# Performance work log

Measured on AMD Instinct MI355X. Metric: run time of the kernel, lower is better.

The kernel has to match this reference:

```python
import jax, jax.numpy as jnp
import numpy as np

B, S, D, H, F, E, K = 2, 2048, 1024, 16, 4096, 8, 2


def setup_inputs() -> dict:
    key = jax.random.key(0)
    ks = jax.random.split(key, 10)
    s = 0.02
    return {
        "x": jax.random.normal(ks[0], (B, S, D), jnp.float32),
        "ln_g": jnp.ones((D,), jnp.float32),
        "ln_b": jnp.zeros((D,), jnp.float32),
        "Wq": s * jax.random.normal(ks[1], (D, D), jnp.float32),
        "Wk": s * jax.random.normal(ks[2], (D, D), jnp.float32),
        "Wv": s * jax.random.normal(ks[3], (D, D), jnp.float32),
        "Wo": s * jax.random.normal(ks[4], (D, D), jnp.float32),
        "Wg": s * jax.random.normal(ks[5], (D, E), jnp.float32),
        "W1": s * jax.random.normal(ks[6], (E, D, F), jnp.float32),
        "b1": jnp.zeros((E, F), jnp.float32),
        "W2": s * jax.random.normal(ks[7], (E, F, D), jnp.float32),
        "b2": jnp.zeros((E, D), jnp.float32),
    }


def _layernorm(x, g, b, eps=1e-5):
    m = x.mean(-1, keepdims=True)
    v = x.var(-1, keepdims=True)
    return (x - m) * jax.lax.rsqrt(v + eps) * g + b


def reference(x, ln_g, ln_b, Wq, Wk, Wv, Wo, Wg, W1, b1, W2, b2):
    Bb, Ss, Dd = x.shape
    dh = Dd // H
    # --- pre-norm multi-head self-attention with residual ---
    h = _layernorm(x, ln_g, ln_b)
    q = (h @ Wq).reshape(Bb, Ss, H, dh)
    k = (h @ Wk).reshape(Bb, Ss, H, dh)
    v = (h @ Wv).reshape(Bb, Ss, H, dh)
    scores = jnp.einsum("bqhd,bkhd->bhqk", q, k) / np.sqrt(dh).astype(np.float32)
    attn = jax.nn.softmax(scores, axis=-1)
    o = jnp.einsum("bhqk,bkhd->bqhd", attn, v).reshape(Bb, Ss, Dd) @ Wo
    x = x + o
    # --- top-2 MoE with residual ---
    nE = Wg.shape[-1]
    probs = jax.nn.softmax(x @ Wg, axis=-1)  # [B,S,E]
    topv, topi = jax.lax.top_k(probs, K)
    topv = topv / topv.sum(-1, keepdims=True)
    w = (jax.nn.one_hot(topi, nE, dtype=x.dtype) * topv[..., None]).sum(-2)  # [B,S,E]
    h1 = jax.nn.gelu(jnp.einsum("bsd,edf->besf", x, W1) + b1[None, :, None, :])
    h2 = jnp.einsum("besf,efd->besd", h1, W2) + b2[None, :, None, :]
    out = x + jnp.einsum("bse,besd->bsd", w, h2)
    return out
```

## Files before the change

kernel.cpp:

```cpp
#include <hip/hip_runtime.h>
#include <hip/hip_bf16.h>

constexpr int Sc = 2048;
constexpr int Dc = 1024;
constexpr int Fc = 4096;
constexpr int Ec = 8;
constexpr int NTOK = 4096;

typedef __attribute__((ext_vector_type(8))) short short8;
typedef __attribute__((ext_vector_type(4))) float floatx4;
typedef unsigned short u16;

__device__ __forceinline__ u16 f2bf(float f) {
    __hip_bfloat16 h = __float2bfloat16(f);
    return *reinterpret_cast<u16*>(&h);
}

__device__ __forceinline__ float gelu_fast(float x) {
    float x2 = x * x;
    float z = x * fmaf(-0.07135481282f, x2, -1.5957691216057308f);
    float e = __expf(z);
    return x * __builtin_amdgcn_rcpf(1.0f + e);
}

__device__ __forceinline__ void async16(const u16* g, u16* l) {
    __builtin_amdgcn_global_load_lds(
        (const __attribute__((address_space(1))) unsigned int*)g,
        (__attribute__((address_space(3))) unsigned int*)l, 16, 0, 0);
}

#define BAR() asm volatile("s_barrier" ::: "memory")

__global__ __launch_bounds__(256) void tcast_kernel(const float* __restrict__ src,
                                                    u16* __restrict__ dst,
                                                    int R, int C,
                                                    size_t sstride, size_t dstride) {
    __shared__ float t[64][65];
    const float* s = src + (size_t)blockIdx.z * sstride;
    u16* d = dst + (size_t)blockIdx.z * dstride;
    int r0 = blockIdx.y * 64, c0 = blockIdx.x * 64;
    int tid = threadIdx.x;
#pragma unroll
    for (int i = 0; i < 4; i++) {
        int c = tid + i * 256;
        int row = c >> 4, col4 = (c & 15) * 4;
        float4 v = *(const float4*)(s + (size_t)(r0 + row) * C + c0 + col4);
        t[row][col4 + 0] = v.x;
        t[row][col4 + 1] = v.y;
        t[row][col4 + 2] = v.z;
        t[row][col4 + 3] = v.w;
    }
    __syncthreads();
#pragma unroll
    for (int i = 0; i < 2; i++) {
        int c = tid + i * 256;
        int dr = c >> 3, m8 = (c & 7) * 8;
        union { u16 us[8]; uint4 v; } pk;
#pragma unroll
        for (int j = 0; j < 8; j++) pk.us[j] = f2bf(t[m8 + j][dr]);
        *(uint4*)(d + (size_t)(c0 + dr) * R + r0 + m8) = pk.v;
    }
}

__global__ __launch_bounds__(256) void btrans_kernel(const u16* __restrict__ src,
                                                     u16* __restrict__ dst,
                                                     int R, int C) {
    __shared__ u16 t[64][72];
    int r0 = blockIdx.y * 64, c0 = blockIdx.x * 64;
    int tid = threadIdx.x;
#pragma unroll
    for (int i = 0; i < 2; i++) {
        int c = tid + i * 256;
        int row = c >> 3, s8 = (c & 7) * 8;
        *(uint4*)&t[row][s8] = *(const uint4*)(src + (size_t)(r0 + row) * C + c0 + s8);
    }
    __syncthreads();
#pragma unroll
    for (int i = 0; i < 2; i++) {
        int c = tid + i * 256;
        int row = c >> 3, s8 = (c & 7) * 8;
        union { u16 us[8]; uint4 v; } pk;
#pragma unroll
        for (int j = 0; j < 8; j++) pk.us[j] = t[s8 + j][row];
        *(uint4*)(dst + (size_t)(c0 + row) * R + r0 + s8) = pk.v;
    }
}

__global__ __launch_bounds__(256) void ln_kernel(const float* __restrict__ x,
                                                 const float* __restrict__ g,
                                                 const float* __restrict__ b,
                                                 u16* __restrict__ hb) {
    int row = blockIdx.x, tid = threadIdx.x;
    const float* xr = x + (size_t)row * Dc;
    float4 xv = ((const float4*)xr)[tid];
    float s = xv.x + xv.y + xv.z + xv.w;
    float ss = xv.x * xv.x + xv.y * xv.y + xv.z * xv.z + xv.w * xv.w;
    __shared__ float r1[256], r2[256];
    r1[tid] = s; r2[tid] = ss;
    __syncthreads();
    for (int off = 128; off > 0; off >>= 1) {
        if (tid < off) { r1[tid] += r1[tid + off]; r2[tid] += r2[tid + off]; }
        __syncthreads();
    }
    float mean = r1[0] * (1.0f / Dc);
    float var = r2[0] * (1.0f / Dc) - mean * mean;
    float rs = rsqrtf(var + 1e-5f);
    float4 gv = ((const float4*)g)[tid];
    float4 bv = ((const float4*)b)[tid];
    ushort4 o;
    o.x = f2bf((xv.x - mean) * rs * gv.x + bv.x);
    o.y = f2bf((xv.y - mean) * rs * gv.y + bv.y);
    o.z = f2bf((xv.z - mean) * rs * gv.z + bv.z);
    o.w = f2bf((xv.w - mean) * rs * gv.w + bv.w);
    *(ushort4*)(hb + (size_t)row * Dc + tid * 4) = o;
}

template <int MODE>
__global__ __launch_bounds__(256) void gemm_mfma(
    const u16* __restrict__ A, const u16* __restrict__ BT,
    int N, int K,
    u16* __restrict__ out_q, u16* __restrict__ out_k, u16* __restrict__ out_v,
    const float* __restrict__ resid, float* __restrict__ out_f32,
    u16* __restrict__ out_bf, const float* __restrict__ bias,
    const int* __restrict__ counts, const int* __restrict__ offsets,
    const int* __restrict__ list_tok) {
    const int tid = threadIdx.x;
    const int m0 = blockIdx.y * 128, n0 = blockIdx.x * 128;
    __shared__ u16 As[128][32];
    __shared__ u16 Bs[128][32];
    const u16* Bbase = BT;
    const int w = tid >> 6, lane = tid & 63;
    const int wm = (w >> 1) * 64, wn = (w & 1) * 64;
    const int lr = lane & 15, lq = lane >> 4;

    const int rA0 = w * 32 + (lane >> 2), rA1 = rA0 + 16;
    const int gsegu = (((lane & 3) ^ ((lane >> 3) & 3))) * 8;
    size_t ra0 = (size_t)(m0 + rA0) * K;
    size_t ra1 = (size_t)(m0 + rA1) * K;
    const u16* gA0 = A + ra0 + gsegu;
    const u16* gA1 = A + ra1 + gsegu;
    const u16* gB0 = Bbase + (size_t)(n0 + rA0) * K + gsegu;
    const u16* gB1 = Bbase + (size_t)(n0 + rA1) * K + gsegu;
    u16* ldsA0 = &As[w * 32][0];
    u16* ldsA1 = &As[w * 32 + 16][0];
    u16* ldsB0 = &Bs[w * 32][0];
    u16* ldsB1 = &Bs[w * 32 + 16][0];

    const int fs = (lq ^ ((lr >> 1) & 3)) * 8;
    const u16* apt[4];
    const u16* bpt[4];
#pragma unroll
    for (int i = 0; i < 4; i++) {
        apt[i] = &As[wm + i * 16 + lr][fs];
        bpt[i] = &Bs[wn + i * 16 + lr][fs];
    }

    floatx4 acc[4][4];
#pragma unroll
    for (int i = 0; i < 4; i++)
#pragma unroll
        for (int j = 0; j < 4; j++) acc[i][j] = (floatx4){0.f, 0.f, 0.f, 0.f};

    for (int k0 = 0; k0 < K; k0 += 32) {
        async16(gA0 + k0, ldsA0);
        async16(gA1 + k0, ldsA1);
        async16(gB0 + k0, ldsB0);
        async16(gB1 + k0, ldsB1);
        __syncthreads();
        short8 af[4], bfr[4];
#pragma unroll
        for (int i = 0; i < 4; i++) af[i] = *(const short8*)apt[i];
#pragma unroll
        for (int j = 0; j < 4; j++) bfr[j] = *(const short8*)bpt[j];
#pragma unroll
        for (int i = 0; i < 4; i++)
#pragma unroll
            for (int j = 0; j < 4; j++)
                acc[i][j] = __builtin_amdgcn_mfma_f32_16x16x32_bf16(af[i], bfr[j], acc[i][j], 0, 0, 0);
        __syncthreads();
    }

#pragma unroll
    for (int i = 0; i < 4; i++)
#pragma unroll
        for (int j = 0; j < 4; j++) {
            int col = n0 + wn + j * 16 + lr;
            int row0 = m0 + wm + i * 16 + lq * 4;
#pragma unroll
            for (int r = 0; r < 4; r++) {
                size_t idx = (size_t)(row0 + r) * 1024 + col;
                float v = acc[i][j][r] + resid[idx];
                out_f32[idx] = v;
                out_bf[idx] = f2bf(v);
            }
        }
}

template <int MODE>
__global__ __launch_bounds__(512, 2) void gemm256(
    const u16* __restrict__ A, const u16* __restrict__ BT, int Nn, int Kfull,
    u16* __restrict__ out_q, u16* __restrict__ out_k, u16* __restrict__ out_v,
    u16* __restrict__ out_bf, float* __restrict__ o32a, float* __restrict__ o32b,
    const float* __restrict__ bias,
    const int* __restrict__ counts, const int* __restrict__ offsets,
    const int* __restrict__ list_tok) {
    __shared__ __attribute__((aligned(16))) u16 smem[66048];
    int e = 0, cnt = 0, off = 0, ks = 0;
    const int bm = (int)blockIdx.y;
    const int bn = (int)blockIdx.x;
    if (MODE >= 2) {
        e = (MODE == 3) ? ((int)blockIdx.z >> 1) : (int)blockIdx.z;
        if (MODE == 3) ks = (int)blockIdx.z & 1;
        cnt = counts[e];
        if (bm * 256 >= cnt) return;
        off = offsets[e];
    }
    const int tid = threadIdx.x;
    const int m0 = bm * 256, n0 = bn * 256;
    const int w = tid >> 6, lane = tid & 63;
    const int wm = w >> 2, wn = w & 3;
    const int lr = lane & 15, lq = lane >> 4;
    const int sz8 = (lr & 7) << 3;

    int* toksL = (int*)(smem + 65536);
    if (MODE == 2) {
        if (tid < 256) toksL[tid] = list_tok[off + min(m0 + tid, cnt - 1)];
        __syncthreads();
    }
    const int K = Kfull;
    const int NT = (MODE == 3 ? 2048 : K) / 64;
    const size_t kb = (MODE == 3) ? (size_t)ks * 2048 : 0;
    const u16* Bb = BT + (MODE >= 2 ? (size_t)e * (size_t)Nn * K : (size_t)0);

    const u16* srcA[4];
    const u16* srcB[4];
    {
        const int rl8 = w * 8 + (lane >> 3);
        const int sg = ((lane & 7) ^ (lane >> 3)) * 8;
#pragma unroll
        for (int i = 0; i < 4; i++) {
            int rA = i * 64 + rl8;
            size_t gr;
            if (MODE == 2) gr = (size_t)toksL[rA];
            else if (MODE == 3) gr = (size_t)(off + min(m0 + rA, cnt - 1));
            else gr = (size_t)(m0 + rA);
            srcA[i] = A + gr * K + kb + sg;
            srcB[i] = Bb + (size_t)(n0 + rA) * K + kb + sg;
        }
    }

    short8 areg[4][2], breg[4][2];
    floatx4 acc[8][4];
#pragma unroll
    for (int i = 0; i < 8; i++)
#pragma unroll
        for (int j = 0; j < 4; j++) acc[i][j] = (floatx4){0.f, 0.f, 0.f, 0.f};

#define STG(kt, mat, h)                                                            \
    do {                                                                           \
        u16* _ld = smem + ((kt) & 1) * 32768 + (mat) * 16384 + (h) * 8192 + w * 512; \
        async16(((mat) ? srcB : srcA)[(h) * 2 + 0] + (size_t)(kt) * 64, _ld);      \
        async16(((mat) ? srcB : srcA)[(h) * 2 + 1] + (size_t)(kt) * 64, _ld + 4096); \
    } while (0)

    auto ldA = [&](int bufp, int mq) {
        const u16* ah = smem + bufp * 32768 + wm * 8192 + (mq * 64 + lr) * 64;
#pragma unroll
        for (int mf = 0; mf < 4; mf++)
#pragma unroll
            for (int kk = 0; kk < 2; kk++)
                areg[mf][kk] = *(const short8*)(ah + mf * 1024 + ((kk * 32 + lq * 8) ^ sz8));
    };
    const int bBo = 16384 + (wn >> 1) * 8192 + (wn & 1) * 4096 + lr * 64;
    auto ldB01 = [&](int bufp) {
        const u16* bh = smem + bufp * 32768 + bBo;
#pragma unroll
        for (int kk = 0; kk < 2; kk++) {
            breg[0][kk] = *(const short8*)(bh + ((kk * 32 + lq * 8) ^ sz8));
            breg[1][kk] = *(const short8*)(bh + 1024 + ((kk * 32 + lq * 8) ^ sz8));
        }
    };
    auto ldB23 = [&](int bufp) {
        const u16* bh = smem + bufp * 32768 + bBo;
#pragma unroll
        for (int kk = 0; kk < 2; kk++) {
            breg[2][kk] = *(const short8*)(bh + 2048 + ((kk * 32 + lq * 8) ^ sz8));
            breg[3][kk] = *(const short8*)(bh + 3072 + ((kk * 32 + lq * 8) ^ sz8));
        }
    };

#define MMQ(MB, NB)                                                                  \
    do {                                                                             \
        __builtin_amdgcn_s_setprio(1);                                               \
        _Pragma("unroll") for (int kk = 0; kk < 2; kk++) {                           \
            _Pragma("unroll") for (int mi = 0; mi < 4; mi++) {                       \
                acc[(MB) + mi][(NB) + 0] = __builtin_amdgcn_mfma_f32_16x16x32_bf16(  \
                    areg[mi][kk], breg[(NB) + 0][kk], acc[(MB) + mi][(NB) + 0], 0, 0, 0); \
                acc[(MB) + mi][(NB) + 1] = __builtin_amdgcn_mfma_f32_16x16x32_bf16(  \
                    areg[mi][kk], breg[(NB) + 1][kk], acc[(MB) + mi][(NB) + 1], 0, 0, 0); \
            }                                                                        \
        }                                                                            \
        __builtin_amdgcn_s_setprio(0);                                               \
    } while (0)

    STG(0, 1, 0); STG(0, 0, 0); STG(0, 0, 1); STG(0, 1, 1);
    STG(1, 1, 0); STG(1, 0, 0);

    for (int t = 0; t < NT; ++t) {
        const int bp = t & 1;
        if (t + 1 < NT) STG(t + 1, 0, 1);
        if (t == NT - 1) { asm volatile("s_waitcnt vmcnt(0)" ::: "memory"); }
        else             { asm volatile("s_waitcnt vmcnt(6)" ::: "memory"); }
        BAR();
        ldA(bp, 0);
        ldB01(bp);
        MMQ(0, 0);
        BAR();
        ldB23(bp);
        if (t + 1 < NT) STG(t + 1, 1, 1);
        BAR();
        MMQ(0, 2);
        BAR();
        ldA(bp, 1);
        if (t + 2 < NT) STG(t + 2, 1, 0);
        BAR();
        MMQ(4, 0);
        BAR();
        if (t + 2 < NT) STG(t + 2, 0, 0);
        BAR();
        MMQ(4, 2);
        BAR();
    }
#undef STG
#undef MMQ

    if (MODE == 0 || MODE == 2) {
#pragma unroll
        for (int nj = 0; nj < 4; nj++) {
            const int colg = wn * 64 + nj * 16 + lr;
            const float bv = (MODE == 2) ? bias[(size_t)e * 4096 + n0 + colg] : 0.f;
            const int g = colg >> 3, rem = colg & 7;
#pragma unroll
            for (int fi = 0; fi < 8; fi++) {
#pragma unroll
                for (int r = 0; r < 4; r++) {
                    const int row = wm * 128 + fi * 16 + lq * 4 + r;
                    float v = acc[fi][nj][r];
                    if (MODE == 2) v = gelu_fast(v + bv);
                    const int pg = (g & ~7) | ((g ^ row) & 7);
                    smem[row * 256 + pg * 8 + rem] = f2bf(v);
                }
            }
        }
        __syncthreads();
        const int mat = n0 >> 10;
        u16* dst0 = (MODE == 0) ? ((mat == 0) ? out_q : (mat == 1 ? out_k : out_v)) : out_bf;
#pragma unroll
        for (int p = 0; p < 16; p++) {
            const int f = tid + p * 512;
            const int row = f >> 5, g = f & 31;
            const int pg = (g & ~7) | ((g ^ row) & 7);
            const uint4 val = *(const uint4*)&smem[row * 256 + pg * 8];
            if (MODE == 0) {
                const int cc = (n0 + g * 8) & 1023;
                *(uint4*)&dst0[(size_t)(m0 + row) * 1024 + cc] = val;
            } else {
                if (m0 + row < cnt)
                    *(uint4*)&dst0[(size_t)(off + m0 + row) * 4096 + n0 + g * 8] = val;
            }
        }
    } else if (MODE == 3) {
        float* o = ks ? o32b : o32a;
#pragma unroll
        for (int nj = 0; nj < 4; nj++) {
            const int col = n0 + wn * 64 + nj * 16 + lr;
            const float bv = ks ? 0.f : bias[(size_t)e * 1024 + col];
#pragma unroll
            for (int fi = 0; fi < 8; fi++) {
                const int rl0 = m0 + wm * 128 + fi * 16 + lq * 4;
#pragma unroll
                for (int r = 0; r < 4; r++)
                    if (rl0 + r < cnt)
                        o[(size_t)(off + rl0 + r) * 1024 + col] = acc[fi][nj][r] + bv;
            }
        }
    }
}

__global__ __launch_bounds__(256) void attn_mfma(const u16* __restrict__ qb,
                                                 const u16* __restrict__ kb,
                                                 const u16* __restrict__ vt,
                                                 u16* __restrict__ aob) {
    __shared__ u16 qs[64][72], ks[64][72], vs[64][72], ps[64][72];
    const int q0 = blockIdx.x * 64, h = blockIdx.y, b = blockIdx.z;
    const int tid = threadIdx.x, w = tid >> 6, lane = tid & 63;
    const int lr = lane & 15, lq = lane >> 4;
    const int ms = w * 16;
    const size_t tok0 = (size_t)b * Sc;

#pragma unroll
    for (int i = 0; i < 2; i++) {
        int c = tid + i * 256;
        int row = c >> 3, d8 = (c & 7) * 8;
        *(uint4*)&qs[row][d8] = *(const uint4*)(qb + (tok0 + q0 + row) * 1024 + h * 64 + d8);
    }
    __syncthreads();
    short8 qa[2];
    qa[0] = *(const short8*)&qs[ms + lr][lq * 8];
    qa[1] = *(const short8*)&qs[ms + lr][32 + lq * 8];

    floatx4 oacc[4];
    float m_r[4], l_r[4];
#pragma unroll
    for (int d4 = 0; d4 < 4; d4++) oacc[d4] = (floatx4){0.f, 0.f, 0.f, 0.f};
#pragma unroll
    for (int r = 0; r < 4; r++) { m_r[r] = -1e30f; l_r[r] = 0.f; }

    for (int kt = 0; kt < Sc / 64; kt++) {
        int k0 = kt * 64;
        __syncthreads();
#pragma unroll
        for (int i = 0; i < 2; i++) {
            int c = tid + i * 256;
            int row = c >> 3, d8 = (c & 7) * 8;
            *(uint4*)&ks[row][d8] = *(const uint4*)(kb + (tok0 + k0 + row) * 1024 + h * 64 + d8);
            *(uint4*)&vs[row][d8] = *(const uint4*)(vt + (size_t)(h * 64 + row) * 4096 + tok0 + k0 + d8);
        }
        __syncthreads();
        floatx4 sfr[4];
#pragma unroll
        for (int j4 = 0; j4 < 4; j4++) {
            short8 kf0 = *(const short8*)&ks[j4 * 16 + lr][lq * 8];
            short8 kf1 = *(const short8*)&ks[j4 * 16 + lr][32 + lq * 8];
            floatx4 sa = (floatx4){0.f, 0.f, 0.f, 0.f};
            sa = __builtin_amdgcn_mfma_f32_16x16x32_bf16(qa[0], kf0, sa, 0, 0, 0);
            sa = __builtin_amdgcn_mfma_f32_16x16x32_bf16(qa[1], kf1, sa, 0, 0, 0);
            sfr[j4] = sa * 0.125f;
        }
#pragma unroll
        for (int r = 0; r < 4; r++) {
            float mx = fmaxf(fmaxf(sfr[0][r], sfr[1][r]), fmaxf(sfr[2][r], sfr[3][r]));
            mx = fmaxf(mx, __shfl_xor(mx, 1, 64));
            mx = fmaxf(mx, __shfl_xor(mx, 2, 64));
            mx = fmaxf(mx, __shfl_xor(mx, 4, 64));
            mx = fmaxf(mx, __shfl_xor(mx, 8, 64));
            float mn = fmaxf(m_r[r], mx);
            float alpha = __expf(m_r[r] - mn);
            m_r[r] = mn;
            float rs = 0.f;
#pragma unroll
            for (int j4 = 0; j4 < 4; j4++) {
                float p = __expf(sfr[j4][r] - mn);
                sfr[j4][r] = p;
                rs += p;
            }
            rs += __shfl_xor(rs, 1, 64);
            rs += __shfl_xor(rs, 2, 64);
            rs += __shfl_xor(rs, 4, 64);
            rs += __shfl_xor(rs, 8, 64);
            l_r[r] = l_r[r] * alpha + rs;
#pragma unroll
            for (int d4 = 0; d4 < 4; d4++) oacc[d4][r] *= alpha;
        }
#pragma unroll
        for (int j4 = 0; j4 < 4; j4++)
#pragma unroll
            for (int r = 0; r < 4; r++)
                ps[ms + lq * 4 + r][j4 * 16 + lr] = f2bf(sfr[j4][r]);
        __syncthreads();
        short8 pa0 = *(const short8*)&ps[ms + lr][lq * 8];
        short8 pa1 = *(const short8*)&ps[ms + lr][32 + lq * 8];
#pragma unroll
        for (int d4 = 0; d4 < 4; d4++) {
            short8 vf0 = *(const short8*)&vs[d4 * 16 + lr][lq * 8];
            short8 vf1 = *(const short8*)&vs[d4 * 16 + lr][32 + lq * 8];
            oacc[d4] = __builtin_amdgcn_mfma_f32_16x16x32_bf16(pa0, vf0, oacc[d4], 0, 0, 0);
            oacc[d4] = __builtin_amdgcn_mfma_f32_16x16x32_bf16(pa1, vf1, oacc[d4], 0, 0, 0);
        }
    }
#pragma unroll
    for (int r = 0; r < 4; r++) {
        float inv = 1.0f / l_r[r];
#pragma unroll
        for (int d4 = 0; d4 < 4; d4++)
            ps[ms + lq * 4 + r][d4 * 16 + lr] = f2bf(oacc[d4][r] * inv);
    }
    __syncthreads();
#pragma unroll
    for (int p = 0; p < 2; p++) {
        int f = tid + p * 256;
        int row = f >> 3, g = f & 7;
        uint4 v = *(const uint4*)&ps[row][g * 8];
        *(uint4*)&aob[(tok0 + q0 + row) * 1024 + h * 64 + g * 8] = v;
    }
}

__global__ __launch_bounds__(256) void router_kernel(const float* __restrict__ x2,
                                                     const float* __restrict__ Wg,
                                                     int* __restrict__ topi,
                                                     float* __restrict__ topw,
                                                     int* __restrict__ counts) {
    int t = blockIdx.x, tid = threadIdx.x;
    float p[Ec] = {};
    const float* xr = x2 + (size_t)t * Dc;
    for (int k = tid; k < Dc; k += 256) {
        float xv = xr[k];
        const float* wr = Wg + (size_t)k * Ec;
#pragma unroll
        for (int e = 0; e < Ec; e++) p[e] += xv * wr[e];
    }
    __shared__ float red[256 * Ec];
#pragma unroll
    for (int e = 0; e < Ec; e++) red[tid * Ec + e] = p[e];
    __syncthreads();
    for (int off = 128; off > 0; off >>= 1) {
        if (tid < off) {
#pragma unroll
            for (int e = 0; e < Ec; e++) red[tid * Ec + e] += red[(tid + off) * Ec + e];
        }
        __syncthreads();
    }
    if (tid == 0) {
        float l[Ec];
        float mx = -1e30f;
#pragma unroll
        for (int e = 0; e < Ec; e++) { l[e] = red[e]; mx = fmaxf(mx, l[e]); }
#pragma unroll
        for (int e = 0; e < Ec; e++) l[e] = __expf(l[e] - mx);
        int i0 = 0;
#pragma unroll
        for (int e = 1; e < Ec; e++) if (l[e] > l[i0]) i0 = e;
        int i1 = (i0 == 0) ? 1 : 0;
#pragma unroll
        for (int e = 0; e < Ec; e++) if (e != i0 && l[e] > l[i1]) i1 = e;
        float v0 = l[i0], v1 = l[i1];
        float inv = 1.0f / (v0 + v1);
        topi[t * 2 + 0] = i0;
        topi[t * 2 + 1] = i1;
        topw[t * 2 + 0] = v0 * inv;
        topw[t * 2 + 1] = v1 * inv;
        atomicAdd(&counts[i0], 1);
        atomicAdd(&counts[i1], 1);
    }
}

__global__ void zero_small(int* counts, int* cursor) {
    int i = threadIdx.x;
    if (i < Ec) { counts[i] = 0; cursor[i] = 0; }
}

__global__ void scan_kernel(const int* counts, int* offsets) {
    if (threadIdx.x == 0) {
        int s = 0;
        for (int e = 0; e < Ec; e++) { offsets[e] = s; s += counts[e]; }
    }
}

__global__ __launch_bounds__(256) void scatter_kernel(const int* __restrict__ topi,
                                                      const int* __restrict__ offsets,
                                                      int* __restrict__ cursor,
                                                      int* __restrict__ list_tok,
                                                      int* __restrict__ slot_of) {
    int t = blockIdx.x * 256 + threadIdx.x;
    if (t >= NTOK) return;
    for (int s2 = 0; s2 < 2; s2++) {
        int e = topi[t * 2 + s2];
        int p = offsets[e] + atomicAdd(&cursor[e], 1);
        list_tok[p] = t;
        slot_of[t * 2 + s2] = p;
    }
}

__global__ __launch_bounds__(256) void combine_kernel(const float* __restrict__ x2,
                                                      const float* __restrict__ h2a,
                                                      const float* __restrict__ h2b,
                                                      const int* __restrict__ slot_of,
                                                      const float* __restrict__ topw,
                                                      float* __restrict__ out) {
    int t = blockIdx.x, c = threadIdx.x;
    int s0 = slot_of[t * 2], s1 = slot_of[t * 2 + 1];
    float w0 = topw[t * 2], w1 = topw[t * 2 + 1];
    float4 a = ((const float4*)(x2 + (size_t)t * Dc))[c];
    float4 p0 = ((const float4*)(h2a + (size_t)s0 * Dc))[c];
    float4 q0 = ((const float4*)(h2b + (size_t)s0 * Dc))[c];
    float4 p1 = ((const float4*)(h2a + (size_t)s1 * Dc))[c];
    float4 q1 = ((const float4*)(h2b + (size_t)s1 * Dc))[c];
    float4 o;
    o.x = a.x + w0 * (p0.x + q0.x) + w1 * (p1.x + q1.x);
    o.y = a.y + w0 * (p0.y + q0.y) + w1 * (p1.y + q1.y);
    o.z = a.z + w0 * (p0.z + q0.z) + w1 * (p1.z + q1.z);
    o.w = a.w + w0 * (p0.w + q0.w) + w1 * (p1.w + q1.w);
    ((float4*)(out + (size_t)t * Dc))[c] = o;
}

extern "C" void kernel_launch(void* const* d_in, const int* in_sizes, int n_in,
                              void* d_out, int out_size, void* d_ws, size_t ws_size,
                              hipStream_t stream) {
    const float* x    = (const float*)d_in[0];
    const float* ln_g = (const float*)d_in[1];
    const float* ln_b = (const float*)d_in[2];
    const float* Wq   = (const float*)d_in[3];
    const float* Wk   = (const float*)d_in[4];
    const float* Wv   = (const float*)d_in[5];
    const float* Wo   = (const float*)d_in[6];
    const float* Wg   = (const float*)d_in[7];
    const float* W1   = (const float*)d_in[8];
    const float* b1   = (const float*)d_in[9];
    const float* W2   = (const float*)d_in[10];
    const float* b2   = (const float*)d_in[11];
    float* out = (float*)d_out;

    char* ws = (char*)d_ws;
    const size_t MB = 1ull << 20;
    float* x2    = (float*)(ws + 0 * MB);
    u16* x2b     = (u16*)(ws + 16 * MB);
    u16* hb      = (u16*)(ws + 24 * MB);
    u16* wqkvT   = (u16*)(ws + 32 * MB);
    u16* woT     = (u16*)(ws + 38 * MB);
    u16* qb      = (u16*)(ws + 40 * MB);
    u16* kb      = (u16*)(ws + 48 * MB);
    u16* vt      = (u16*)(ws + 56 * MB);
    u16* vb      = (u16*)(ws + 64 * MB);
    u16* aob     = (u16*)(ws + 64 * MB);
    float* h2b   = (float*)(ws + 40 * MB);
    u16* w1T     = (u16*)(ws + 72 * MB);
    u16* w2T     = (u16*)(ws + 136 * MB);
    u16* h1      = (u16*)(ws + 200 * MB);
    float* h2    = (float*)(ws + 264 * MB);
    char* sm     = ws + 296 * MB;
    float* topw    = (float*)(sm);
    int*   topi    = (int*)(sm + (1 << 15));
    int*   slot_of = (int*)(sm + 2 * (1 << 15));
    int*   list_tok= (int*)(sm + 3 * (1 << 15));
    int*   counts  = (int*)(sm + 4 * (1 << 15));
    int*   offsets = counts + 64;
    int*   cursor  = counts + 128;

    tcast_kernel<<<dim3(16, 16, 1), 256, 0, stream>>>(Wq, wqkvT + 0 * 1024 * 1024, 1024, 1024, 0, 0);
    tcast_kernel<<<dim3(16, 16, 1), 256, 0, stream>>>(Wk, wqkvT + 1 * 1024 * 1024, 1024, 1024, 0, 0);
    tcast_kernel<<<dim3(16, 16, 1), 256, 0, stream>>>(Wv, wqkvT + 2 * 1024 * 1024, 1024, 1024, 0, 0);
    tcast_kernel<<<dim3(16, 16, 1), 256, 0, stream>>>(Wo, woT, 1024, 1024, 0, 0);
    tcast_kernel<<<dim3(64, 16, 8), 256, 0, stream>>>(W1, w1T, 1024, 4096,
                                                      (size_t)1024 * 4096, (size_t)4096 * 1024);
    tcast_kernel<<<dim3(16, 64, 8), 256, 0, stream>>>(W2, w2T, 4096, 1024,
                                                      (size_t)4096 * 1024, (size_t)1024 * 4096);

    ln_kernel<<<NTOK, 256, 0, stream>>>(x, ln_g, ln_b, hb);
    gemm256<0><<<dim3(12, 16, 1), 512, 0, stream>>>(hb, wqkvT, 3072, 1024,
                                                    qb, kb, vb, nullptr, nullptr, nullptr,
                                                    nullptr, nullptr, nullptr, nullptr);
    btrans_kernel<<<dim3(16, 64), 256, 0, stream>>>(vb, vt, 4096, 1024);
    attn_mfma<<<dim3(Sc / 64, 16, 2), 256, 0, stream>>>(qb, kb, vt, aob);
    gemm_mfma<1><<<dim3(8, 32), 256, 0, stream>>>(aob, woT, 1024, 1024,
                                                  nullptr, nullptr, nullptr, x, x2, x2b, nullptr,
                                                  nullptr, nullptr, nullptr);

    zero_small<<<1, 64, 0, stream>>>(counts, cursor);
    router_kernel<<<NTOK, 256, 0, stream>>>(x2, Wg, topi, topw, counts);
    scan_kernel<<<1, 1, 0, stream>>>(counts, offsets);
    scatter_kernel<<<NTOK / 256, 256, 0, stream>>>(topi, offsets, cursor, list_tok, slot_of);

    gemm256<2><<<dim3(16, 16, 8), 512, 0, stream>>>(x2b, w1T, 4096, 1024,
                                                    nullptr, nullptr, nullptr,
                                                    h1, nullptr, nullptr, b1,
                                                    counts, offsets, list_tok);
    gemm256<3><<<dim3(4, 16, 16), 512, 0, stream>>>(h1, w2T, 1024, 4096,
                                                    nullptr, nullptr, nullptr,
                                                    nullptr, h2, h2b, b2,
                                                    counts, offsets, list_tok);
    combine_kernel<<<NTOK, 256, 0, stream>>>(x2, h2, h2b, slot_of, topw, out);
}
```

Measured before the change: 949.8 us.

## Relax GEMM barriers and double-buffer K/V tiles in attention

The MoE GEMM main loop now issues the next-stage async global-to-LDS copies earlier, waits on fewer outstanding vector loads, and replaces several workgroup barriers with per-wave lgkmcnt waits plus scheduling barriers. The attention kernel now double-buffers the K/V tiles in LDS. It prefetches the next tile into registers while computing on the current one and drops one of the two __syncthreads per key tile. The aim is to cut barrier stalls and hide global load latency behind MFMA work. The cost is more LDS and registers in attention, and a possible LDS race in the GEMM if a wave overwrites a buffer that another wave is still reading.

New measurement: 918.3 us. 1.03x faster.

```diff
diff --git a/kernel.cpp b/kernel.cpp
--- a/kernel.cpp
+++ b/kernel.cpp
@@ -30,6 +30,11 @@
 }
 
 #define BAR() asm volatile("s_barrier" ::: "memory")
+#define LGKM0_SGB()                                            \
+    do {                                                       \
+        asm volatile("s_waitcnt lgkmcnt(0)" ::: "memory");     \
+        __builtin_amdgcn_sched_barrier(0);                     \
+    } while (0)
 
 __global__ __launch_bounds__(256) void tcast_kernel(const float* __restrict__ src,
                                                     u16* __restrict__ dst,
@@ -308,28 +313,25 @@
 
     for (int t = 0; t < NT; ++t) {
         const int bp = t & 1;
-        if (t + 1 < NT) STG(t + 1, 0, 1);
         if (t == NT - 1) { asm volatile("s_waitcnt vmcnt(0)" ::: "memory"); }
-        else             { asm volatile("s_waitcnt vmcnt(6)" ::: "memory"); }
+        else             { asm volatile("s_waitcnt vmcnt(4)" ::: "memory"); }
         BAR();
         ldA(bp, 0);
         ldB01(bp);
+        if (t + 1 < NT) STG(t + 1, 0, 1);
+        LGKM0_SGB();
+        ldB23(bp);
         MMQ(0, 0);
-        BAR();
-        ldB23(bp);
         if (t + 1 < NT) STG(t + 1, 1, 1);
-        BAR();
+        LGKM0_SGB();
         MMQ(0, 2);
         BAR();
         ldA(bp, 1);
         if (t + 2 < NT) STG(t + 2, 1, 0);
-        BAR();
+        LGKM0_SGB();
         MMQ(4, 0);
-        BAR();
         if (t + 2 < NT) STG(t + 2, 0, 0);
-        BAR();
         MMQ(4, 2);
-        BAR();
     }
 #undef STG
 #undef MMQ
@@ -391,19 +393,21 @@
                                                  const u16* __restrict__ kb,
                                                  const u16* __restrict__ vt,
                                                  u16* __restrict__ aob) {
-    __shared__ u16 qs[64][72], ks[64][72], vs[64][72], ps[64][72];
+    __shared__ u16 qs[64][72], ks[2][64][72], vs[2][64][72], ps[64][72];
     const int q0 = blockIdx.x * 64, h = blockIdx.y, b = blockIdx.z;
     const int tid = threadIdx.x, w = tid >> 6, lane = tid & 63;
     const int lr = lane & 15, lq = lane >> 4;
     const int ms = w * 16;
     const size_t tok0 = (size_t)b * Sc;
-
-#pragma unroll
-    for (int i = 0; i < 2; i++) {
-        int c = tid + i * 256;
-        int row = c >> 3, d8 = (c & 7) * 8;
-        *(uint4*)&qs[row][d8] = *(const uint4*)(qb + (tok0 + q0 + row) * 1024 + h * 64 + d8);
-    }
+    const int r0 = tid >> 3, d8 = (tid & 7) * 8;
+    const int r1 = (tid + 256) >> 3;
+
+    *(uint4*)&qs[r0][d8] = *(const uint4*)(qb + (tok0 + q0 + r0) * 1024 + h * 64 + d8);
+    *(uint4*)&qs[r1][d8] = *(const uint4*)(qb + (tok0 + q0 + r1) * 1024 + h * 64 + d8);
+    *(uint4*)&ks[0][r0][d8] = *(const uint4*)(kb + (tok0 + r0) * 1024 + h * 64 + d8);
+    *(uint4*)&ks[0][r1][d8] = *(const uint4*)(kb + (tok0 + r1) * 1024 + h * 64 + d8);
+    *(uint4*)&vs[0][r0][d8] = *(const uint4*)(vt + (size_t)(h * 64 + r0) * 4096 + tok0 + d8);
+    *(uint4*)&vs[0][r1][d8] = *(const uint4*)(vt + (size_t)(h * 64 + r1) * 4096 + tok0 + d8);
     __syncthreads();
     short8 qa[2];
     qa[0] = *(const short8*)&qs[ms + lr][lq * 8];
@@ -416,22 +420,23 @@
 #pragma unroll
     for (int r = 0; r < 4; r++) { m_r[r] = -1e30f; l_r[r] = 0.f; }
 
+    int cur = 0;
     for (int kt = 0; kt < Sc / 64; kt++) {
-        int k0 = kt * 64;
-        __syncthreads();
-#pragma unroll
-        for (int i = 0; i < 2; i++) {
-            int c = tid + i * 256;
-            int row = c >> 3, d8 = (c & 7) * 8;
-            *(uint4*)&ks[row][d8] = *(const uint4*)(kb + (tok0 + k0 + row) * 1024 + h * 64 + d8);
-            *(uint4*)&vs[row][d8] = *(const uint4*)(vt + (size_t)(h * 64 + row) * 4096 + tok0 + k0 + d8);
-        }
-        __syncthreads();
+        if (kt > 0) __syncthreads();
+        uint4 krg0, krg1, vrg0, vrg1;
+        const bool more = (kt + 1 < Sc / 64);
+        if (more) {
+            const int k1 = (kt + 1) * 64;
+            krg0 = *(const uint4*)(kb + (tok0 + k1 + r0) * 1024 + h * 64 + d8);
+            krg1 = *(const uint4*)(kb + (tok0 + k1 + r1) * 1024 + h * 64 + d8);
+            vrg0 = *(const uint4*)(vt + (size_t)(h * 64 + r0) * 4096 + tok0 + k1 + d8);
+            vrg1 = *(const uint4*)(vt + (size_t)(h * 64 + r1) * 4096 + tok0 + k1 + d8);
+        }
         floatx4 sfr[4];
 #pragma unroll
         for (int j4 = 0; j4 < 4; j4++) {
-            short8 kf0 = *(const short8*)&ks[j4 * 16 + lr][lq * 8];
-            short8 kf1 = *(const short8*)&ks[j4 * 16 + lr][32 + lq * 8];
+            short8 kf0 = *(const short8*)&ks[cur][j4 * 16 + lr][lq * 8];
+            short8 kf1 = *(const short8*)&ks[cur][j4 * 16 + lr][32 + lq * 8];
             floatx4 sa = (floatx4){0.f, 0.f, 0.f, 0.f};
             sa = __builtin_amdgcn_mfma_f32_16x16x32_bf16(qa[0], kf0, sa, 0, 0, 0);
             sa = __builtin_amdgcn_mfma_f32_16x16x32_bf16(qa[1], kf1, sa, 0, 0, 0);
@@ -467,16 +472,22 @@
 #pragma unroll
             for (int r = 0; r < 4; r++)
                 ps[ms + lq * 4 + r][j4 * 16 + lr] = f2bf(sfr[j4][r]);
-        __syncthreads();
         short8 pa0 = *(const short8*)&ps[ms + lr][lq * 8];
         short8 pa1 = *(const short8*)&ps[ms + lr][32 + lq * 8];
 #pragma unroll
         for (int d4 = 0; d4 < 4; d4++) {
-            short8 vf0 = *(const short8*)&vs[d4 * 16 + lr][lq * 8];
-            short8 vf1 = *(const short8*)&vs[d4 * 16 + lr][32 + lq * 8];
+            short8 vf0 = *(const short8*)&vs[cur][d4 * 16 + lr][lq * 8];
+            short8 vf1 = *(const short8*)&vs[cur][d4 * 16 + lr][32 + lq * 8];
             oacc[d4] = __builtin_amdgcn_mfma_f32_16x16x32_bf16(pa0, vf0, oacc[d4], 0, 0, 0);
             oacc[d4] = __builtin_amdgcn_mfma_f32_16x16x32_bf16(pa1, vf1, oacc[d4], 0, 0, 0);
         }
+        if (more) {
+            *(uint4*)&ks[cur ^ 1][r0][d8] = krg0;
+            *(uint4*)&ks[cur ^ 1][r1][d8] = krg1;
+            *(uint4*)&vs[cur ^ 1][r0][d8] = vrg0;
+            *(uint4*)&vs[cur ^ 1][r1][d8] = vrg1;
+        }
+        cur ^= 1;
     }
 #pragma unroll
     for (int r = 0; r < 4; r++) {
```
